# Optimization experiments

Measured on AMD Instinct MI355X. Metric: run time of the kernel, lower is better.

## Reference

```python
import jax, jax.numpy as jnp
import numpy as np

D = 1024
B, S = 4, 2048


def setup_inputs() -> dict:
    key = jax.random.key(0)
    ks = jax.random.split(key, 6)
    sc = 1.0 / np.sqrt(D)  # truncated-normal-ish fan-in scale like hk.Linear default
    return {
        "x": jax.random.normal(ks[0], (B, S, D), dtype=jnp.float32),
        "W_amp1": jax.random.normal(ks[1], (D, D), dtype=jnp.float32) * sc,
        "b_amp1": jnp.zeros((D,), dtype=jnp.float32),
        "W_amp2": jax.random.normal(ks[2], (D, D), dtype=jnp.float32) * sc,
        "b_amp2": jnp.zeros((D,), dtype=jnp.float32),
        "vqc_params": jax.random.uniform(ks[3], (D, 4), dtype=jnp.float32, minval=-np.pi, maxval=np.pi),
        "W_post1": jax.random.normal(ks[4], (D, D), dtype=jnp.float32) * sc,
        "b_post1": jnp.zeros((D,), dtype=jnp.float32),
        "W_post2": jax.random.normal(ks[5], (D, D), dtype=jnp.float32) * sc,
        "b_post2": jnp.zeros((D,), dtype=jnp.float32),
    }


def reference(x, W_amp1, b_amp1, W_amp2, b_amp2, vqc_params,
              W_post1, b_post1, W_post2, b_post2):
    # amplitude encoder: Linear -> tanh -> Linear
    amp = jnp.tanh(x @ W_amp1 + b_amp1) @ W_amp2 + b_amp2  # [B,S,D]

    # variational quantum circuit, vectorized over channels:
    # per-channel i: out_i = amp_i*cos(theta_i/2) + Re(amp_i*sin(theta_i/2)*e^{i phi_i})
    #              = amp_i * (cos(theta_i/2) + sin(theta_i/2)*cos(phi_i))
    theta = vqc_params[:, 0]  # [D]
    phi = vqc_params[:, 1]    # [D]
    scale = jnp.cos(theta * 0.5) + jnp.sin(theta * 0.5) * jnp.cos(phi)  # [D]
    q = amp * scale  # broadcast over [B,S,D]

    # classical post: Linear -> silu -> Linear
    out = jax.nn.silu(q @ W_post1 + b_post1) @ W_post2 + b_post2
    return out
```

## Files before the change

### kernel.cpp

```cpp
#include <hip/hip_runtime.h>
#include <hip/hip_bf16.h>
#include <math.h>

#define DD 1024
#define MM 8192

typedef __attribute__((ext_vector_type(8))) short short8;
typedef __attribute__((ext_vector_type(4))) float f32x4;

__device__ inline unsigned short f32_to_bf16(float f) {
  union { float f; unsigned u; } v; v.f = f;
  unsigned u = v.u;
  u += 0x7FFFu + ((u >> 16) & 1u);
  return (unsigned short)(u >> 16);
}

__global__ void k_convert_x(const float4* __restrict__ x, ushort4* __restrict__ o, int n4) {
  int i = blockIdx.x * blockDim.x + threadIdx.x;
  int stride = gridDim.x * blockDim.x;
  for (; i < n4; i += stride) {
    float4 v = x[i];
    ushort4 r;
    r.x = f32_to_bf16(v.x); r.y = f32_to_bf16(v.y);
    r.z = f32_to_bf16(v.z); r.w = f32_to_bf16(v.w);
    o[i] = r;
  }
}

__global__ void k_transpose_w(const float* __restrict__ w0, const float* __restrict__ w1,
                              const float* __restrict__ w2, const float* __restrict__ w3,
                              unsigned short* __restrict__ o0, unsigned short* __restrict__ o1,
                              unsigned short* __restrict__ o2, unsigned short* __restrict__ o3) {
  const float* src; unsigned short* dst;
  switch (blockIdx.z) {
    case 0: src = w0; dst = o0; break;
    case 1: src = w1; dst = o1; break;
    case 2: src = w2; dst = o2; break;
    default: src = w3; dst = o3; break;
  }
  __shared__ float t[32][33];
  int tx = threadIdx.x, ty = threadIdx.y;
  int c0 = blockIdx.x * 32, r0 = blockIdx.y * 32;
  #pragma unroll
  for (int i = 0; i < 4; i++)
    t[ty + 8 * i][tx] = src[(size_t)(r0 + ty + 8 * i) * DD + c0 + tx];
  __syncthreads();
  #pragma unroll
  for (int i = 0; i < 4; i++)
    dst[(size_t)(c0 + ty + 8 * i) * DD + r0 + tx] = f32_to_bf16(t[tx][ty + 8 * i]);
}

__global__ void k_scale(const float* __restrict__ vqc, float* __restrict__ sc) {
  int d = blockIdx.x * blockDim.x + threadIdx.x;
  if (d < DD) {
    float th = vqc[d * 4 + 0] * 0.5f, ph = vqc[d * 4 + 1];
    sc[d] = cosf(th) + sinf(th) * cosf(ph);
  }
}

template <int EPI>
__global__ void k_gemm(const unsigned short* __restrict__ A,
                       const unsigned short* __restrict__ Bt,
                       const float* __restrict__ bias,
                       const float* __restrict__ scale,
                       void* __restrict__ Cout) {
  constexpr int K = DD, N = DD;
  __shared__ unsigned short As[128 * 32];
  __shared__ unsigned short Bs[128 * 32];
  const int tid = threadIdx.x;
  const int wave = tid >> 6, lane = tid & 63;
  const int wr = wave >> 1, wc = wave & 1;
  const int rowA0 = blockIdx.y * 128, colB0 = blockIdx.x * 128;
  const int lr = lane & 15, lk = (lane >> 4) * 8;
  const int seg = wave * 2;
  const int srow = lane >> 2;
  const int skc = (lane & 3) * 8;

  f32x4 acc[4][4] = {};

  for (int k0 = 0; k0 < K; k0 += 32) {
    #pragma unroll
    for (int i = 0; i < 2; i++) {
      int s = seg + i;
      const unsigned short* ga = A + (size_t)(rowA0 + s * 16 + srow) * K + k0 + skc;
      __builtin_amdgcn_global_load_lds(
          (const __attribute__((address_space(1))) unsigned int*)ga,
          (__attribute__((address_space(3))) unsigned int*)(As + s * 512), 16, 0, 0);
      const unsigned short* gb = Bt + (size_t)(colB0 + s * 16 + srow) * K + k0 + skc;
      __builtin_amdgcn_global_load_lds(
          (const __attribute__((address_space(1))) unsigned int*)gb,
          (__attribute__((address_space(3))) unsigned int*)(Bs + s * 512), 16, 0, 0);
    }
    __syncthreads();

    short8 a[4], b[4];
    #pragma unroll
    for (int m = 0; m < 4; m++)
      a[m] = *(const short8*)(As + (wr * 64 + m * 16 + lr) * 32 + lk);
    #pragma unroll
    for (int n = 0; n < 4; n++)
      b[n] = *(const short8*)(Bs + (wc * 64 + n * 16 + lr) * 32 + lk);
    #pragma unroll
    for (int m = 0; m < 4; m++)
      #pragma unroll
      for (int n = 0; n < 4; n++)
        acc[m][n] = __builtin_amdgcn_mfma_f32_16x16x32_bf16(a[m], b[n], acc[m][n], 0, 0, 0);
    __syncthreads();
  }

  const int row0 = rowA0 + wr * 64;
  const int col0 = colB0 + wc * 64;
  #pragma unroll
  for (int n = 0; n < 4; n++) {
    const int col = col0 + n * 16 + lr;
    const float bv = bias[col];
    const float sv = (EPI == 1) ? scale[col] : 0.f;
    #pragma unroll
    for (int m = 0; m < 4; m++) {
      #pragma unroll
      for (int j = 0; j < 4; j++) {
        int row = row0 + m * 16 + (lane >> 4) * 4 + j;
        float z = acc[m][n][j] + bv;
        if constexpr (EPI == 0) {
          ((unsigned short*)Cout)[(size_t)row * N + col] = f32_to_bf16(tanhf(z));
        } else if constexpr (EPI == 1) {
          ((unsigned short*)Cout)[(size_t)row * N + col] = f32_to_bf16(z * sv);
        } else if constexpr (EPI == 2) {
          ((unsigned short*)Cout)[(size_t)row * N + col] = f32_to_bf16(z / (1.f + __expf(-z)));
        } else {
          ((float*)Cout)[(size_t)row * N + col] = z;
        }
      }
    }
  }
}

extern "C" void kernel_launch(void* const* d_in, const int* in_sizes, int n_in,
                              void* d_out, int out_size, void* d_ws, size_t ws_size,
                              hipStream_t stream) {
  const float* x   = (const float*)d_in[0];
  const float* W1  = (const float*)d_in[1];
  const float* b1  = (const float*)d_in[2];
  const float* W2  = (const float*)d_in[3];
  const float* b2  = (const float*)d_in[4];
  const float* vqc = (const float*)d_in[5];
  const float* Wp1 = (const float*)d_in[6];
  const float* bp1 = (const float*)d_in[7];
  const float* Wp2 = (const float*)d_in[8];
  const float* bp2 = (const float*)d_in[9];

  char* ws = (char*)d_ws;
  unsigned short* actA = (unsigned short*)ws;
  unsigned short* actB = (unsigned short*)(ws + (16u << 20));
  unsigned short* Wt0  = (unsigned short*)(ws + (32u << 20));
  unsigned short* Wt1  = (unsigned short*)(ws + (34u << 20));
  unsigned short* Wt2  = (unsigned short*)(ws + (36u << 20));
  unsigned short* Wt3  = (unsigned short*)(ws + (38u << 20));
  float* scale = (float*)(ws + (40u << 20));

  k_convert_x<<<2048, 256, 0, stream>>>((const float4*)x, (ushort4*)actA, MM * DD / 4);
  k_transpose_w<<<dim3(32, 32, 4), dim3(32, 8), 0, stream>>>(W1, W2, Wp1, Wp2, Wt0, Wt1, Wt2, Wt3);
  k_scale<<<4, 256, 0, stream>>>(vqc, scale);

  dim3 g(DD / 128, MM / 128), b(256);
  k_gemm<0><<<g, b, 0, stream>>>(actA, Wt0, b1,  nullptr, actB);
  k_gemm<1><<<g, b, 0, stream>>>(actB, Wt1, b2,  scale,   actA);
  k_gemm<2><<<g, b, 0, stream>>>(actA, Wt2, bp1, nullptr, actB);
  k_gemm<3><<<g, b, 0, stream>>>(actB, Wt3, bp2, nullptr, d_out);
}
```

Measured before the change: 144.1 us.

## Double K-tile depth, XOR-swizzle LDS layout, and remap blocks for L2 locality

The GEMM K-step grows from 32 to 64, which halves the number of barrier pairs per tile and issues two MFMA sub-steps per load phase. The LDS tile gets an XOR swizzle on 16-byte chunks, applied through the global source address of the global_load_lds writes, to cut bank conflicts on the fragment reads. Block indices are remapped into groups of 8 row-tiles sharing column tiles to improve L2 reuse. LDS use per block doubles, which may reduce occupancy.

```diff
diff --git a/kernel.cpp b/kernel.cpp
--- a/kernel.cpp
+++ b/kernel.cpp
@@ -65,46 +65,57 @@
                        const float* __restrict__ scale,
                        void* __restrict__ Cout) {
   constexpr int K = DD, N = DD;
-  __shared__ unsigned short As[128 * 32];
-  __shared__ unsigned short Bs[128 * 32];
+  __shared__ unsigned short As[128 * 64];
+  __shared__ unsigned short Bs[128 * 64];
   const int tid = threadIdx.x;
   const int wave = tid >> 6, lane = tid & 63;
   const int wr = wave >> 1, wc = wave & 1;
-  const int rowA0 = blockIdx.y * 128, colB0 = blockIdx.x * 128;
+
+  const int L = blockIdx.y * gridDim.x + blockIdx.x;
+  const int bx = (L >> 3) & 7;
+  const int by = (L & 7) | ((L >> 6) << 3);
+  const int rowA0 = by * 128, colB0 = bx * 128;
+
   const int lr = lane & 15, lk = (lane >> 4) * 8;
-  const int seg = wave * 2;
-  const int srow = lane >> 2;
-  const int skc = (lane & 3) * 8;
+  const int srow = lane >> 3;
+  const int sswz = ((lane & 7) ^ srow) * 8;
 
   f32x4 acc[4][4] = {};
 
-  for (int k0 = 0; k0 < K; k0 += 32) {
+  for (int k0 = 0; k0 < K; k0 += 64) {
     #pragma unroll
-    for (int i = 0; i < 2; i++) {
-      int s = seg + i;
-      const unsigned short* ga = A + (size_t)(rowA0 + s * 16 + srow) * K + k0 + skc;
+    for (int i = 0; i < 4; i++) {
+      int r = wave * 32 + i * 8;
+      const unsigned short* ga = A + (size_t)(rowA0 + r + srow) * K + k0 + sswz;
       __builtin_amdgcn_global_load_lds(
           (const __attribute__((address_space(1))) unsigned int*)ga,
-          (__attribute__((address_space(3))) unsigned int*)(As + s * 512), 16, 0, 0);
-      const unsigned short* gb = Bt + (size_t)(colB0 + s * 16 + srow) * K + k0 + skc;
+          (__attribute__((address_space(3))) unsigned int*)(As + r * 64), 16, 0, 0);
+      const unsigned short* gb = Bt + (size_t)(colB0 + r + srow) * K + k0 + sswz;
       __builtin_amdgcn_global_load_lds(
           (const __attribute__((address_space(1))) unsigned int*)gb,
-          (__attribute__((address_space(3))) unsigned int*)(Bs + s * 512), 16, 0, 0);
+          (__attribute__((address_space(3))) unsigned int*)(Bs + r * 64), 16, 0, 0);
     }
     __syncthreads();
 
-    short8 a[4], b[4];
     #pragma unroll
-    for (int m = 0; m < 4; m++)
-      a[m] = *(const short8*)(As + (wr * 64 + m * 16 + lr) * 32 + lk);
-    #pragma unroll
-    for (int n = 0; n < 4; n++)
-      b[n] = *(const short8*)(Bs + (wc * 64 + n * 16 + lr) * 32 + lk);
-    #pragma unroll
-    for (int m = 0; m < 4; m++)
+    for (int kk = 0; kk < 64; kk += 32) {
+      short8 a[4], b[4];
       #pragma unroll
-      for (int n = 0; n < 4; n++)
-        acc[m][n] = __builtin_amdgcn_mfma_f32_16x16x32_bf16(a[m], b[n], acc[m][n], 0, 0, 0);
+      for (int m = 0; m < 4; m++) {
+        int row = wr * 64 + m * 16 + lr;
+        a[m] = *(const short8*)(As + row * 64 + (((((kk + lk) >> 3)) ^ (row & 7)) << 3));
+      }
+      #pragma unroll
+      for (int n = 0; n < 4; n++) {
+        int row = wc * 64 + n * 16 + lr;
+        b[n] = *(const short8*)(Bs + row * 64 + (((((kk + lk) >> 3)) ^ (row & 7)) << 3));
+      }
+      #pragma unroll
+      for (int m = 0; m < 4; m++)
+        #pragma unroll
+        for (int n = 0; n < 4; n++)
+          acc[m][n] = __builtin_amdgcn_mfma_f32_16x16x32_bf16(a[m], b[n], acc[m][n], 0, 0, 0);
+    }
     __syncthreads();
   }
 
```

New measurement: 118.8 us. 1.21x faster.
